# Performance work log

Measured on AMD Instinct MI355X. Metric: run time of the kernel, lower is better.

The kernel has to match this reference:

```python
import jax, jax.numpy as jnp
import numpy as np

# pywt 'haar': dec_lo = [1/sqrt2, 1/sqrt2], dec_hi = [-1/sqrt2, 1/sqrt2]
_SQ = np.float32(1.0 / np.sqrt(2.0))
_DEC_LO = np.array([_SQ, _SQ], dtype=np.float32)
_DEC_HI = np.array([-_SQ, _SQ], dtype=np.float32)


def _make_filter():
    ll = np.outer(_DEC_LO, _DEC_LO)
    lh = np.outer(_DEC_HI, _DEC_LO)
    hl = np.outer(_DEC_LO, _DEC_HI)
    hh = np.outer(_DEC_HI, _DEC_HI)
    # torch code writes filters flipped ([::-1, ::-1]) then uses cross-correlation
    f = np.stack([ll, lh, hl, hh], axis=0)[:, ::-1, ::-1]  # [4, 2, 2]
    return jnp.asarray(np.ascontiguousarray(f))


def setup_inputs() -> dict:
    key = jax.random.key(0)
    x = jax.random.normal(key, (8, 64, 256, 256), dtype=jnp.float32)
    return {"x": x}


def reference(x):
    B, C, H, W = x.shape
    filt = _make_filter()  # [4, 2, 2]
    # The torch module's split/pad/conv3d/split/cat pipeline is equivalent to a
    # depthwise 2x2 conv producing 4 subbands per channel, ordered
    # [c0:(LL,LH,HL,HH), c1:(LL,LH,HL,HH), ...] along the channel dim.
    kernel = jnp.tile(filt[None], (C, 1, 1, 1)).reshape(C * 4, 1, 2, 2)
    # F.pad(..., (0,1,0,1)): pad right and bottom by 1 with zeros
    xp = jnp.pad(x, ((0, 0), (0, 0), (0, 1), (0, 1)))
    out = jax.lax.conv_general_dilated(
        xp, kernel,
        window_strides=(1, 1),
        padding='VALID',
        dimension_numbers=('NCHW', 'OIHW', 'NCHW'),
        feature_group_count=C,
    )
    return out  # [B, 4*C, H, W]
```

## Files before the change

kernel.cpp:

```cpp
#include <hip/hip_runtime.h>


typedef float f32x4 __attribute__((ext_vector_type(4)));

constexpr int Bn = 8, Cn = 64, Hn = 256, Wn = 256;
constexpr int ROWS_PER_WAVE   = 4;
constexpr int WAVES_PER_BLOCK = 4;
constexpr int ROWS_PER_BLOCK  = ROWS_PER_WAVE * WAVES_PER_BLOCK;

__global__ __launch_bounds__(256)
void haar_dwt_kernel(const float* __restrict__ x, float* __restrict__ out) {
    const int tid  = threadIdx.x;
    const int lane = tid & 63;
    const int wv   = tid >> 6;

    const int bc   = blockIdx.y;
    const int row0 = blockIdx.x * ROWS_PER_BLOCK + wv * ROWS_PER_WAVE;
    const int j0   = lane * 4;

    const size_t plane_elems = (size_t)Hn * Wn;
    const float* p = x + (size_t)bc * plane_elems + (size_t)row0 * Wn + j0;

    f32x4 r[ROWS_PER_WAVE + 1];
    float e[ROWS_PER_WAVE + 1];
    const bool has_e = (j0 + 4 < Wn);

#pragma unroll
    for (int k = 0; k < ROWS_PER_WAVE; ++k) {
        const float* pk = p + k * Wn;
        r[k] = *reinterpret_cast<const f32x4*>(pk);
        e[k] = has_e ? pk[4] : 0.0f;
    }
    {
        const f32x4 zero4 = {0.f, 0.f, 0.f, 0.f};
        f32x4 rl = zero4;
        float el = 0.0f;
        if (row0 + ROWS_PER_WAVE < Hn) {
            const float* pk = p + ROWS_PER_WAVE * Wn;
            rl = *reinterpret_cast<const f32x4*>(pk);
            el = has_e ? pk[4] : 0.0f;
        }
        r[ROWS_PER_WAVE] = rl;
        e[ROWS_PER_WAVE] = el;
    }

    float* obase = out + (size_t)(4 * bc) * plane_elems + (size_t)row0 * Wn + j0;

#pragma unroll
    for (int i = 0; i < ROWS_PER_WAVE; ++i) {
        const float a0[5] = {r[i][0], r[i][1], r[i][2], r[i][3], e[i]};
        const float a1[5] = {r[i+1][0], r[i+1][1], r[i+1][2], r[i+1][3], e[i+1]};

        f32x4 vll, vlh, vhl, vhh;
#pragma unroll
        for (int k = 0; k < 4; ++k) {
            const float sum0 = a0[k] + a0[k + 1];
            const float dif0 = a0[k] - a0[k + 1];
            const float sum1 = a1[k] + a1[k + 1];
            const float dif1 = a1[k] - a1[k + 1];
            vll[k] = 0.5f * (sum0 + sum1);
            vlh[k] = 0.5f * (sum0 - sum1);
            vhl[k] = 0.5f * (dif0 + dif1);
            vhh[k] = 0.5f * (dif0 - dif1);
        }

        float* orow = obase + i * Wn;
        __builtin_nontemporal_store(vll, reinterpret_cast<f32x4*>(orow));
        __builtin_nontemporal_store(vlh, reinterpret_cast<f32x4*>(orow + plane_elems));
        __builtin_nontemporal_store(vhl, reinterpret_cast<f32x4*>(orow + 2 * plane_elems));
        __builtin_nontemporal_store(vhh, reinterpret_cast<f32x4*>(orow + 3 * plane_elems));
    }
}

extern "C" void kernel_launch(void* const* d_in, const int* in_sizes, int n_in,
                              void* d_out, int out_size, void* d_ws, size_t ws_size,
                              hipStream_t stream) {
    const float* x = (const float*)d_in[0];
    float* out = (float*)d_out;

    dim3 grid(Hn / ROWS_PER_BLOCK, Bn * Cn);
    haar_dwt_kernel<<<grid, 256, 0, stream>>>(x, out);
}
```

Measured before the change: 616.3 us.

## Use persistent grid-stride kernel with shuffle-based edge reads and load prefetch

```diff
diff --git a/kernel.cpp b/kernel.cpp
--- a/kernel.cpp
+++ b/kernel.cpp
@@ -4,52 +4,51 @@
 typedef float f32x4 __attribute__((ext_vector_type(4)));
 
 constexpr int Bn = 8, Cn = 64, Hn = 256, Wn = 256;
-constexpr int ROWS_PER_WAVE   = 4;
-constexpr int WAVES_PER_BLOCK = 4;
-constexpr int ROWS_PER_BLOCK  = ROWS_PER_WAVE * WAVES_PER_BLOCK;
+constexpr int TPB    = 256;
+constexpr int BLOCKS = 2048;
+constexpr int PLANE  = Hn * Wn;
+constexpr int TOTAL_THREADS = BLOCKS * TPB;
+constexpr int ITEMS  = Bn * Cn * Hn * (Wn / 4);
+constexpr int ITERS  = ITEMS / TOTAL_THREADS;
+constexpr int BC_STRIDE = TOTAL_THREADS / (Hn * (Wn / 4));
 
-__global__ __launch_bounds__(256)
+__global__ __launch_bounds__(TPB)
 void haar_dwt_kernel(const float* __restrict__ x, float* __restrict__ out) {
-    const int tid  = threadIdx.x;
-    const int lane = tid & 63;
-    const int wv   = tid >> 6;
+    const int g    = blockIdx.x * TPB + threadIdx.x;
+    const int lane = threadIdx.x & 63;
+    const int row  = (g >> 6) & (Hn - 1);
+    const int bc0  = g >> 14;
+    const int j0   = (g & 63) * 4;
 
-    const int bc   = blockIdx.y;
-    const int row0 = blockIdx.x * ROWS_PER_BLOCK + wv * ROWS_PER_WAVE;
-    const int j0   = lane * 4;
+    const bool has_row1 = (row + 1 < Hn);
+    const bool has_e    = (lane != 63);
 
-    const size_t plane_elems = (size_t)Hn * Wn;
-    const float* p = x + (size_t)bc * plane_elems + (size_t)row0 * Wn + j0;
+    const float* p = x   + (size_t)bc0 * PLANE       + (size_t)row * Wn + j0;
+    float*       o = out + (size_t)(4 * bc0) * PLANE + (size_t)row * Wn + j0;
 
-    f32x4 r[ROWS_PER_WAVE + 1];
-    float e[ROWS_PER_WAVE + 1];
-    const bool has_e = (j0 + 4 < Wn);
+    const size_t in_step  = (size_t)BC_STRIDE * PLANE;
+    const size_t out_step = (size_t)BC_STRIDE * 4 * PLANE;
 
-#pragma unroll
-    for (int k = 0; k < ROWS_PER_WAVE; ++k) {
-        const float* pk = p + k * Wn;
-        r[k] = *reinterpret_cast<const f32x4*>(pk);
-        e[k] = has_e ? pk[4] : 0.0f;
-    }
-    {
-        const f32x4 zero4 = {0.f, 0.f, 0.f, 0.f};
-        f32x4 rl = zero4;
-        float el = 0.0f;
-        if (row0 + ROWS_PER_WAVE < Hn) {
-            const float* pk = p + ROWS_PER_WAVE * Wn;
-            rl = *reinterpret_cast<const f32x4*>(pk);
-            el = has_e ? pk[4] : 0.0f;
+    f32x4 r0 = *reinterpret_cast<const f32x4*>(p);
+    f32x4 r1 = {0.f, 0.f, 0.f, 0.f};
+    if (has_row1) r1 = *reinterpret_cast<const f32x4*>(p + Wn);
+
+    for (int it = 0; it < ITERS; ++it) {
+        const float* pn = p + in_step;
+        f32x4 n0 = {0.f, 0.f, 0.f, 0.f};
+        f32x4 n1 = {0.f, 0.f, 0.f, 0.f};
+        if (it + 1 < ITERS) {
+            n0 = *reinterpret_cast<const f32x4*>(pn);
+            if (has_row1) n1 = *reinterpret_cast<const f32x4*>(pn + Wn);
         }
-        r[ROWS_PER_WAVE] = rl;
-        e[ROWS_PER_WAVE] = el;
-    }
 
-    float* obase = out + (size_t)(4 * bc) * plane_elems + (size_t)row0 * Wn + j0;
+        const float t0 = __shfl_down(r0[0], 1);
+        const float t1 = __shfl_down(r1[0], 1);
+        const float e0 = has_e ? t0 : 0.0f;
+        const float e1 = has_e ? t1 : 0.0f;
 
-#pragma unroll
-    for (int i = 0; i < ROWS_PER_WAVE; ++i) {
-        const float a0[5] = {r[i][0], r[i][1], r[i][2], r[i][3], e[i]};
-        const float a1[5] = {r[i+1][0], r[i+1][1], r[i+1][2], r[i+1][3], e[i+1]};
+        const float a0[5] = {r0[0], r0[1], r0[2], r0[3], e0};
+        const float a1[5] = {r1[0], r1[1], r1[2], r1[3], e1};
 
         f32x4 vll, vlh, vhl, vhh;
 #pragma unroll
@@ -64,11 +63,15 @@
             vhh[k] = 0.5f * (dif0 - dif1);
         }
 
-        float* orow = obase + i * Wn;
-        __builtin_nontemporal_store(vll, reinterpret_cast<f32x4*>(orow));
-        __builtin_nontemporal_store(vlh, reinterpret_cast<f32x4*>(orow + plane_elems));
-        __builtin_nontemporal_store(vhl, reinterpret_cast<f32x4*>(orow + 2 * plane_elems));
-        __builtin_nontemporal_store(vhh, reinterpret_cast<f32x4*>(orow + 3 * plane_elems));
+        *reinterpret_cast<f32x4*>(o)             = vll;
+        *reinterpret_cast<f32x4*>(o + PLANE)     = vlh;
+        *reinterpret_cast<f32x4*>(o + 2 * PLANE) = vhl;
+        *reinterpret_cast<f32x4*>(o + 3 * PLANE) = vhh;
+
+        p = pn;
+        o += out_step;
+        r0 = n0;
+        r1 = n1;
     }
 }
 
@@ -78,6 +81,5 @@
     const float* x = (const float*)d_in[0];
     float* out = (float*)d_out;
 
-    dim3 grid(Hn / ROWS_PER_BLOCK, Bn * Cn);
-    haar_dwt_kernel<<<grid, 256, 0, stream>>>(x, out);
+    haar_dwt_kernel<<<BLOCKS, TPB, 0, stream>>>(x, out);
 }
```

Result: no change. 607.1 us (-1.5%).
